# Performance work log

Measured on AMD Instinct MI355X. Metric: run time of the kernel, lower is better.

## Reference

```python
import jax, jax.numpy as jnp
import numpy as np

DISP_SCALE = (-4.0, -3.0, -2.0, -1.0, 0.0, 1.0, 2.0, 3.0, 4.0)
GROUP_NUM = 8


def _warp_x(feat, disp):
    """Bilinear warp of feat along x by -disp (x_dist=-1, y_dist=0), zero padding.

    feat: [B, C, H, W], disp: [B, 1, H, W]. Samples feat at x' = x - disp.
    """
    B, C, H, W = feat.shape
    xs = jnp.arange(W, dtype=feat.dtype)[None, None, :] - disp[:, 0]  # [B, H, W]
    x0 = jnp.floor(xs)
    w1 = (xs - x0)[:, None]                     # [B, 1, H, W] right-neighbor weight
    x0i = x0.astype(jnp.int32)
    x1i = x0i + 1
    v0 = ((x0i >= 0) & (x0i < W)).astype(feat.dtype)[:, None]  # [B, 1, H, W]
    v1 = ((x1i >= 0) & (x1i < W)).astype(feat.dtype)[:, None]
    x0c = jnp.clip(x0i, 0, W - 1)[:, None]      # [B, 1, H, W]
    x1c = jnp.clip(x1i, 0, W - 1)[:, None]
    g0 = jnp.take_along_axis(feat, jnp.broadcast_to(x0c, (B, C, H, W)), axis=3)
    g1 = jnp.take_along_axis(feat, jnp.broadcast_to(x1c, (B, C, H, W)), axis=3)
    return g0 * ((1.0 - w1) * v0) + g1 * (w1 * v1)


def _group_correlation(feat1, feat2, num_groups):
    B, C, H, W = feat1.shape
    cpg = C // num_groups
    prod = feat1 * feat2
    return prod.reshape(B, num_groups, cpg, H, W).mean(axis=2)  # [B, G, H, W]


def setup_inputs() -> dict:
    key = jax.random.key(0)
    k1, k2, k3 = jax.random.split(key, 3)
    B, C, H, W = 8, 64, 256, 256
    return {
        "feat_left": jax.random.normal(k1, (B, C, H, W), dtype=jnp.float32),
        "feat_right": jax.random.normal(k2, (B, C, H, W), dtype=jnp.float32),
        "disp_init": jax.random.uniform(k3, (B, 1, H, W), dtype=jnp.float32),
    }


def reference(feat_left, feat_right, disp_init):
    # loop over the small fixed hyperparameter list of disparity offsets
    costs = []
    for off in DISP_SCALE:
        disp = disp_init + off
        feat_warp = _warp_x(feat_right, disp)
        costs.append(_group_correlation(feat_left, feat_warp, GROUP_NUM))
    return jnp.stack(costs, axis=2)  # [B, G, disp_num, H, W]
```

## Files before the change

kernel.cpp:

```cpp
#include <hip/hip_runtime.h>

#define WID 256
#define HEI 256
#define CH  64
#define GRP 8
#define CPG 8
#define ND  9

__global__ __launch_bounds__(256, 2)
void cost_volume_kernel(const float* __restrict__ L,
                        const float* __restrict__ R,
                        const float* __restrict__ disp,
                        float* __restrict__ out) {
    __shared__ float sR[CH * WID];

    const int bh  = blockIdx.x;
    const int b   = bh >> 8;
    const int h   = bh & 255;
    const int tid = threadIdx.x;

    {
        const float4* R4 = reinterpret_cast<const float4*>(R);
        float4* s4 = reinterpret_cast<float4*>(sR);
        const size_t bbase4 = (size_t)b * CH * (HEI * WID / 4) + (size_t)h * (WID / 4);
        #pragma unroll
        for (int i = 0; i < 16; ++i) {
            const int idx = tid + i * 256;
            const int c  = idx >> 6;
            const int w4 = idx & 63;
            s4[idx] = R4[bbase4 + (size_t)c * (HEI * WID / 4) + w4];
        }
    }
    __syncthreads();

    const int w = tid;
    const float dv   = disp[((size_t)b * HEI + h) * WID + w];
    const float base = (float)w - dv;
    const float fb   = floorf(base);
    const float frac = base - fb;
    const int   fib  = (int)fb;

    float wl[ND], wr[ND];
    #pragma unroll
    for (int d = 0; d < ND; ++d) {
        const int x0 = fib + 4 - d;
        const int x1 = x0 + 1;
        wl[d] = (x0 >= 0 && x0 < WID) ? (1.0f - frac) : 0.0f;
        wr[d] = (x1 >= 0 && x1 < WID) ? frac : 0.0f;
    }
    const bool interior = (fib >= 4) && (fib <= WID - 6);

    const size_t lbase = (((size_t)b * CH) * HEI + h) * WID + w;

    #pragma unroll 1
    for (int g = 0; g < GRP; ++g) {
        float acc[ND];
        #pragma unroll
        for (int d = 0; d < ND; ++d) acc[d] = 0.0f;

        float lf[CPG];
        #pragma unroll
        for (int k = 0; k < CPG; ++k)
            lf[k] = L[lbase + (size_t)(g * CPG + k) * (HEI * WID)];

        #pragma unroll
        for (int k = 0; k < CPG; ++k) {
            const int c = g * CPG + k;
            float rv[10];
            if (interior) {
                const int rb = c * WID + fib - 4;
                #pragma unroll
                for (int j = 0; j < 10; ++j) rv[j] = sR[rb + j];
            } else {
                #pragma unroll
                for (int j = 0; j < 10; ++j) {
                    int x = fib - 4 + j;
                    x = min(max(x, 0), WID - 1);
                    rv[j] = sR[c * WID + x];
                }
            }
            const float lv = lf[k];
            #pragma unroll
            for (int d = 0; d < ND; ++d)
                acc[d] = fmaf(lv, fmaf(rv[9 - d], wr[d], rv[8 - d] * wl[d]), acc[d]);
        }

        const size_t og = ((size_t)(b * GRP + g) * ND) * (HEI * WID) + (size_t)h * WID + w;
        #pragma unroll
        for (int d = 0; d < ND; ++d)
            out[og + (size_t)d * (HEI * WID)] = acc[d] * 0.125f;
    }
}

extern "C" void kernel_launch(void* const* d_in, const int* in_sizes, int n_in,
                              void* d_out, int out_size, void* d_ws, size_t ws_size,
                              hipStream_t stream) {
    const float* feat_left  = (const float*)d_in[0];
    const float* feat_right = (const float*)d_in[1];
    const float* disp_init  = (const float*)d_in[2];
    float* out = (float*)d_out;

    const int B = 8;
    dim3 grid(B * HEI);
    dim3 block(256);
    cost_volume_kernel<<<grid, block, 0, stream>>>(feat_left, feat_right, disp_init, out);
}
```

Measured before the change: 86.24 us.

## Double-buffer right features per group via async LDS loads and factor disparity weights

Instead of staging all 64 channels of the right row into LDS up front, the kernel stages one 8-channel group at a time. It uses double-buffered global_load_lds, so the next group's load overlaps compute on the current one. This shrinks LDS per block so more blocks can be resident (launch bounds raised to 4). The inner loop accumulates 10 shifted products per group once and applies the bilinear weights only at output time, which cuts FMA count. Outputs use nontemporal stores. The kernel is already close to memory-bandwidth bound, so the overlap and occupancy gains may be small, and it now adds a barrier per group.

```diff
diff --git a/kernel.cpp b/kernel.cpp
--- a/kernel.cpp
+++ b/kernel.cpp
@@ -6,90 +6,103 @@
 #define GRP 8
 #define CPG 8
 #define ND  9
+#define HW  (HEI * WID)
 
-__global__ __launch_bounds__(256, 2)
+__global__ __launch_bounds__(256, 4)
 void cost_volume_kernel(const float* __restrict__ L,
                         const float* __restrict__ R,
                         const float* __restrict__ disp,
                         float* __restrict__ out) {
-    __shared__ float sR[CH * WID];
+    __shared__ float sR[2][CPG * WID];
 
-    const int bh  = blockIdx.x;
-    const int b   = bh >> 8;
-    const int h   = bh & 255;
-    const int tid = threadIdx.x;
+    const int bh   = blockIdx.x;
+    const int b    = bh >> 8;
+    const int h    = bh & 255;
+    const int tid  = threadIdx.x;
+    const int wv   = tid >> 6;
+    const int lane = tid & 63;
 
-    {
-        const float4* R4 = reinterpret_cast<const float4*>(R);
-        float4* s4 = reinterpret_cast<float4*>(sR);
-        const size_t bbase4 = (size_t)b * CH * (HEI * WID / 4) + (size_t)h * (WID / 4);
-        #pragma unroll
-        for (int i = 0; i < 16; ++i) {
-            const int idx = tid + i * 256;
-            const int c  = idx >> 6;
-            const int w4 = idx & 63;
-            s4[idx] = R4[bbase4 + (size_t)c * (HEI * WID / 4) + w4];
-        }
-    }
-    __syncthreads();
+    const float4* R4 = reinterpret_cast<const float4*>(R);
+    const size_t bbase4 = (size_t)b * CH * (HW / 4) + (size_t)h * (WID / 4);
+
+#define STAGE(gidx, bufidx)                                                      \
+    do {                                                                         \
+        _Pragma("unroll")                                                        \
+        for (int i_ = 0; i_ < 2; ++i_) {                                         \
+            const int cc_ = (gidx) * CPG + wv * 2 + i_;                          \
+            const float4* gsrc_ = R4 + bbase4 + (size_t)cc_ * (HW / 4) + lane;   \
+            __builtin_amdgcn_global_load_lds(                                    \
+                (const __attribute__((address_space(1))) void*)gsrc_,            \
+                (__attribute__((address_space(3))) void*)&sR[bufidx][(wv * 2 + i_) * WID], \
+                16, 0, 0);                                                       \
+        }                                                                        \
+    } while (0)
 
     const int w = tid;
-    const float dv   = disp[((size_t)b * HEI + h) * WID + w];
+    const float dv   = disp[(size_t)b * HW + (size_t)h * WID + w];
     const float base = (float)w - dv;
     const float fb   = floorf(base);
     const float frac = base - fb;
     const int   fib  = (int)fb;
-
-    float wl[ND], wr[ND];
-    #pragma unroll
-    for (int d = 0; d < ND; ++d) {
-        const int x0 = fib + 4 - d;
-        const int x1 = x0 + 1;
-        wl[d] = (x0 >= 0 && x0 < WID) ? (1.0f - frac) : 0.0f;
-        wr[d] = (x1 >= 0 && x1 < WID) ? frac : 0.0f;
-    }
     const bool interior = (fib >= 4) && (fib <= WID - 6);
 
-    const size_t lbase = (((size_t)b * CH) * HEI + h) * WID + w;
+    const size_t lbase = ((size_t)b * CH * HEI + h) * WID + w;
+    const size_t obase = ((size_t)(b * GRP) * ND) * HW + (size_t)h * WID + w;
+
+    STAGE(0, 0);
+    __syncthreads();
 
     #pragma unroll 1
     for (int g = 0; g < GRP; ++g) {
-        float acc[ND];
-        #pragma unroll
-        for (int d = 0; d < ND; ++d) acc[d] = 0.0f;
+        if (g + 1 < GRP) STAGE(g + 1, (g + 1) & 1);
 
         float lf[CPG];
         #pragma unroll
         for (int k = 0; k < CPG; ++k)
-            lf[k] = L[lbase + (size_t)(g * CPG + k) * (HEI * WID)];
+            lf[k] = L[lbase + (size_t)(g * CPG + k) * HW];
 
+        const float* sb = sR[g & 1];
+
+        float S[10];
         #pragma unroll
-        for (int k = 0; k < CPG; ++k) {
-            const int c = g * CPG + k;
-            float rv[10];
-            if (interior) {
-                const int rb = c * WID + fib - 4;
+        for (int j = 0; j < 10; ++j) S[j] = 0.0f;
+
+        if (interior) {
+            #pragma unroll
+            for (int k = 0; k < CPG; ++k) {
+                const int rb = k * WID + fib - 4;
+                const float lv = lf[k];
                 #pragma unroll
-                for (int j = 0; j < 10; ++j) rv[j] = sR[rb + j];
-            } else {
+                for (int j = 0; j < 10; ++j)
+                    S[j] = fmaf(lv, sb[rb + j], S[j]);
+            }
+        } else {
+            #pragma unroll
+            for (int k = 0; k < CPG; ++k) {
+                const float lv = lf[k];
                 #pragma unroll
                 for (int j = 0; j < 10; ++j) {
                     int x = fib - 4 + j;
                     x = min(max(x, 0), WID - 1);
-                    rv[j] = sR[c * WID + x];
+                    S[j] = fmaf(lv, sb[k * WID + x], S[j]);
                 }
             }
-            const float lv = lf[k];
-            #pragma unroll
-            for (int d = 0; d < ND; ++d)
-                acc[d] = fmaf(lv, fmaf(rv[9 - d], wr[d], rv[8 - d] * wl[d]), acc[d]);
         }
 
-        const size_t og = ((size_t)(b * GRP + g) * ND) * (HEI * WID) + (size_t)h * WID + w;
+        const size_t og = obase + (size_t)g * ND * HW;
         #pragma unroll
-        for (int d = 0; d < ND; ++d)
-            out[og + (size_t)d * (HEI * WID)] = acc[d] * 0.125f;
+        for (int d = 0; d < ND; ++d) {
+            const int x0 = fib + 4 - d;
+            const int x1 = x0 + 1;
+            const float wl = (x0 >= 0 && x0 < WID) ? (1.0f - frac) : 0.0f;
+            const float wr = (x1 >= 0 && x1 < WID) ? frac : 0.0f;
+            const float v = fmaf(wl, S[8 - d], wr * S[9 - d]) * 0.125f;
+            __builtin_nontemporal_store(v, &out[og + (size_t)d * HW]);
+        }
+
+        __syncthreads();
     }
+#undef STAGE
 }
 
 extern "C" void kernel_launch(void* const* d_in, const int* in_sizes, int n_in,
@@ -100,8 +113,7 @@
     const float* disp_init  = (const float*)d_in[2];
     float* out = (float*)d_out;
 
-    const int B = 8;
-    dim3 grid(B * HEI);
+    dim3 grid(8 * HEI);
     dim3 block(256);
     cost_volume_kernel<<<grid, block, 0, stream>>>(feat_left, feat_right, disp_init, out);
 }
```

After: 70.67 us. 18.1% less time.
